# Optimization experiments

Measured on AMD Instinct MI355X. Metric: run time of the kernel, lower is better.

## Reference

```python
import jax, jax.numpy as jnp
import numpy as np
from functools import partial

MAX_SPAN_WIDTH = 8


def setup_inputs() -> dict:
    key = jax.random.key(0)
    ks = jax.random.split(key, 8)
    B, S, H = 4, 256, 256
    NE, D = 50000, 256  # entity_embedding_dim == hidden_size
    inp = {
        "embeddings": jax.random.normal(ks[0], (B, S, H), jnp.float32),          # BERT outputs[0]
        "entity_table": jax.random.normal(ks[1], (NE, D), jnp.float32) * 0.02,   # nn.Embedding weight
        "span_W": jax.random.normal(ks[2], (2 * H + 1, H), jnp.float32) * 0.02,  # span_embedding Linear
        "span_b": jax.random.normal(ks[3], (H,), jnp.float32) * 0.02,
        "gcn_W1": jax.random.normal(ks[4], (D, H), jnp.float32) * 0.02,
        "gcn_b1": jax.random.normal(ks[5], (H,), jnp.float32) * 0.02,
        "gcn_W2": jax.random.normal(ks[6], (H, H), jnp.float32) * 0.02,
        "gcn_b2": jax.random.normal(ks[7], (H,), jnp.float32) * 0.02,
        "k": 8,
    }
    return inp


def _star_adj_norm(k, dtype):
    # k-node star graph (node 0 hub) with self-loops, symmetric GCN normalization
    A = jnp.zeros((k, k), dtype).at[0, 1:].set(1.0).at[1:, 0].set(1.0) + jnp.eye(k, dtype=dtype)
    deg = A.sum(axis=1)
    return A / jnp.sqrt(deg[:, None] * deg[None, :])


def reference(embeddings, entity_table, span_W, span_b, gcn_W1, gcn_b1, gcn_W2, gcn_b2, k):
    B, S, H = embeddings.shape
    Wmax = MAX_SPAN_WIDTH
    dtype = embeddings.dtype

    # token_inputs: CLS embedding per example
    cls = embeddings[:, 0, :]  # [B, H]

    # Vectorized ragged span max-pool: running max over widths 1..Wmax.
    # span_max[w, b, s, :] = max(embeddings[b, s : s+w+1, :])
    neg_inf = jnp.array(-jnp.inf, dtype)
    maxes = []
    cur = embeddings
    maxes.append(cur)
    for w in range(1, Wmax):
        shifted = jnp.concatenate(
            [embeddings[:, w:, :], jnp.full((B, w, H), neg_inf, dtype)], axis=1)
        cur = jnp.maximum(cur, shifted)  # -inf pad => out-of-range positions ignored
        maxes.append(cur)
    span_max = jnp.stack(maxes, axis=0)  # [Wmax, B, S, H]

    # concat(max-pool, CLS, span width) -> span_embedding Linear
    cls_b = jnp.broadcast_to(cls[None, :, None, :], (Wmax, B, S, H))
    width_feat = jnp.broadcast_to(
        jnp.arange(1, Wmax + 1, dtype=dtype)[:, None, None, None], (Wmax, B, S, 1))
    span_inputs = jnp.concatenate([span_max, cls_b, width_feat], axis=-1)  # [Wmax,B,S,2H+1]
    span_inputs = span_inputs.reshape(Wmax * B * S, 2 * H + 1)             # [N, 2H+1]
    span_repr = span_inputs @ span_W + span_b                              # [N, H]

    # build_subgraph: top-k similar entities per span (memory-bound similarity + top-k)
    sims = span_repr @ entity_table.T          # [N, NE]  ~1.6GB intermediate
    _, topk_idx = jax.lax.top_k(sims, k)       # [N, k]
    node_x = entity_table[topk_idx]            # gather -> [N, k, D]

    # 2-layer GCN on the fixed star subgraph (gather-linear-scatter equivalent)
    A_norm = _star_adj_norm(k, dtype)          # [k, k]
    h = jax.nn.relu(jnp.einsum('ij,njd,dh->nih', A_norm, node_x, gcn_W1) + gcn_b1)
    subgraph_out = jnp.einsum('ij,njd,dh->nih', A_norm, h, gcn_W2) + gcn_b2  # [N, k, H]

    return cls, span_repr, subgraph_out
```

## Files before the change

### kernel.cpp

```cpp
#include <hip/hip_runtime.h>

typedef unsigned short u16;
typedef unsigned int   u32;
typedef unsigned long long u64;
typedef short bf16x8 __attribute__((ext_vector_type(8)));
typedef float f32x4  __attribute__((ext_vector_type(4)));

#define INF_F __builtin_inff()

__device__ __forceinline__ u16 f2bf(float f) {
  u32 u = __float_as_uint(f);
  return (u16)((u + 0x7FFFu + ((u >> 16) & 1u)) >> 16);
}

__device__ __forceinline__ u32 sortf(float f) {
  u32 u = __float_as_uint(f);
  return u ^ ((u32)((int)u >> 31) | 0x80000000u);
}
__device__ __forceinline__ float unsortf(u32 s) {
  u32 u = s ^ ((s & 0x80000000u) ? 0x80000000u : 0xFFFFFFFFu);
  return __uint_as_float(u);
}
__device__ __forceinline__ u64 sx64(u64 v, int m) {
  u32 lo = __shfl_xor((u32)v, m);
  u32 hi = __shfl_xor((u32)(v >> 32), m);
  return ((u64)hi << 32) | lo;
}

__device__ __forceinline__ void gload_lds16(const void* g, void* l) {
  __builtin_amdgcn_global_load_lds(
      (const __attribute__((address_space(1))) u32*)g,
      (__attribute__((address_space(3))) u32*)l, 16, 0, 0);
}

__global__ __launch_bounds__(256) void k0_cvt(
    const float* __restrict__ src, u16* __restrict__ dst, int n4) {
  int id = blockIdx.x * 256 + threadIdx.x;
  if (id >= n4) return;
  float4 v = ((const float4*)src)[id];
  ((ushort4*)dst)[id] = make_ushort4(f2bf(v.x), f2bf(v.y), f2bf(v.z), f2bf(v.w));
}

__global__ __launch_bounds__(256) void k1_span(
    const float* __restrict__ emb, const float* __restrict__ Wsp,
    const float* __restrict__ bsp,
    float* __restrict__ out0, float* __restrict__ out1,
    u16* __restrict__ spanbf) {
  __shared__ float SM[8][256];
  __shared__ float CLS[256];
  const int bid = blockIdx.x;
  const int b = bid >> 8, s = bid & 255;
  const int t = threadIdx.x;
  const float* eb = emb + (size_t)b * 65536;

  CLS[t] = eb[t];
  if (s == 0) out0[b * 256 + t] = eb[t];

  float m = eb[s * 256 + t];
  SM[0][t] = m;
  #pragma unroll
  for (int w = 1; w < 8; ++w) {
    if (s + w < 256) m = fmaxf(m, eb[(s + w) * 256 + t]);
    SM[w][t] = m;
  }
  __syncthreads();

  float cc = 0.f;
  for (int k = 0; k < 256; k += 4) {
    float4 cq = *(const float4*)&CLS[k];
    cc += cq.x * Wsp[(size_t)(256 + k + 0) * 256 + t];
    cc += cq.y * Wsp[(size_t)(256 + k + 1) * 256 + t];
    cc += cq.z * Wsp[(size_t)(256 + k + 2) * 256 + t];
    cc += cq.w * Wsp[(size_t)(256 + k + 3) * 256 + t];
  }
  float acc[8];
  const float base = bsp[t] + cc;
  #pragma unroll
  for (int w = 0; w < 8; ++w) acc[w] = base;

  for (int k = 0; k < 256; k += 4) {
    float w0 = Wsp[(size_t)(k + 0) * 256 + t];
    float w1 = Wsp[(size_t)(k + 1) * 256 + t];
    float w2 = Wsp[(size_t)(k + 2) * 256 + t];
    float w3 = Wsp[(size_t)(k + 3) * 256 + t];
    #pragma unroll
    for (int w = 0; w < 8; ++w) {
      float4 smq = *(const float4*)&SM[w][k];
      acc[w] += smq.x * w0; acc[w] += smq.y * w1;
      acc[w] += smq.z * w2; acc[w] += smq.w * w3;
    }
  }
  const float wm = Wsp[(size_t)512 * 256 + t];
  #pragma unroll
  for (int w = 0; w < 8; ++w) {
    float val = acc[w] + (float)(w + 1) * wm;
    size_t idx = ((size_t)w * 1024 + bid) * 256 + t;
    out1[idx] = val;
    spanbf[idx] = f2bf(val);
  }
}

__global__ __launch_bounds__(128, 2) void k2_mfma(
    const u16* __restrict__ spanbf, const u16* __restrict__ entbf, int ne,
    float* __restrict__ Rpv, int* __restrict__ Rpi) {
  __shared__ u32 Elds[6144];
  __shared__ u64 Q[2][64][16];
  const int t = threadIdx.x, lane = t & 63, wv = t >> 6;
  const int m = lane & 15, q = lane >> 4, q4 = q * 4;
  const int p = blockIdx.x & 15, rg = blockIdx.x >> 4;
  const int psz = (ne + 15) >> 4;
  const int e_start = p * psz;
  const int e_end = min(ne, e_start + psz);
  const int rowbase = rg * 128 + wv * 64;
  const u64 gm = 0xFFFFull << (q * 16);
  const u64 lanelow = (lane == 63) ? 0x7FFFFFFFFFFFFFFFull
                                   : ((1ull << (lane + 1)) - 1) >> 1;
  const u64 gml = gm & lanelow;
  const int row = lane & 15;
  const int ls5 = lane >> 5;

  const u64 KINIT = ((u64)sortf(-INF_F) << 32);
  u64 slot[4][4];
  float myth[4], th[4][4];
  #pragma unroll
  for (int h = 0; h < 4; ++h) {
    myth[h] = -INF_F;
    #pragma unroll
    for (int s = 0; s < 4; ++s) { slot[h][s] = KINIT; th[h][s] = -INF_F; }
  }

  bf16x8 a[4][8];
  #pragma unroll
  for (int h = 0; h < 4; ++h)
    #pragma unroll
    for (int s = 0; s < 8; ++s)
      a[h][s] = *(const bf16x8*)(spanbf
                  + (size_t)(rowbase + h * 16 + m) * 256 + s * 32 + q * 8);

  auto issue = [&](int k, int sl) {
    const int cb = e_start + (k << 4);
    #pragma unroll
    for (int i = 0; i < 4; ++i) {
      int eo = wv * 8 + i * 2 + ls5;
      int e  = (sl << 4) + eo;
      int ge = min(cb + eo, e_end - 1);
      int xoff = ((lane & 31) ^ (e & 31)) << 4;
      gload_lds16((const char*)entbf + (size_t)ge * 512 + xoff,
                  (char*)Elds + (sl << 13) + (wv << 12) + (i << 10));
    }
  };

  const int nch = (e_end - e_start + 15) >> 4;
  int cs = 0;
  issue(0, 0);

  for (int pc = 0; pc < nch; ++pc) {
    int is_ = cs + 1; if (is_ == 3) is_ = 0;
    if (pc + 1 < nch) {
      issue(pc + 1, is_);
      asm volatile("s_waitcnt vmcnt(4)" ::: "memory");
    } else {
      asm volatile("s_waitcnt vmcnt(0)" ::: "memory");
    }
    __builtin_amdgcn_sched_barrier(0);
    __builtin_amdgcn_s_barrier();

    f32x4 acc[4];
    #pragma unroll
    for (int h = 0; h < 4; ++h) acc[h] = (f32x4){0.f, 0.f, 0.f, 0.f};
    const int el = (cs << 4) + m, sw = el & 31, bc = el << 5;
    #pragma unroll
    for (int s = 0; s < 8; ++s) {
      int qq = s * 4 + q;
      bf16x8 bfr = *(const bf16x8*)((const char*)Elds + ((bc | (qq ^ sw)) << 4));
      #pragma unroll
      for (int h = 0; h < 4; ++h)
        acc[h] = __builtin_amdgcn_mfma_f32_16x16x32_bf16(a[h][s], bfr, acc[h], 0, 0, 0);
    }
    const int gent = e_start + (pc << 4) + m;
    const bool valid = gent < e_end;

    #pragma unroll
    for (int h = 0; h < 4; ++h) {
      bool any = valid & ((acc[h][0] > th[h][0]) | (acc[h][1] > th[h][1]) |
                          (acc[h][2] > th[h][2]) | (acc[h][3] > th[h][3]));
      if (!__ballot(any)) continue;
      u64 M[4];
      #pragma unroll
      for (int r = 0; r < 4; ++r) {
        bool hr = valid && (acc[h][r] > th[h][r]);
        M[r] = __ballot(hr);
        if (hr) {
          int pos = (int)__popcll(M[r] & gml);
          Q[wv][h * 16 + q4 + r][pos ^ (q4 + r)] =
              ((u64)sortf(acc[h][r]) << 32) | (u32)(~(u32)gent);
        }
      }
      u64 msk = (row & 2) ? ((row & 1) ? M[3] : M[2])
                          : ((row & 1) ? M[1] : M[0]);
      int cnt = (int)__popcll((msk >> ((row >> 2) << 4)) & 0xFFFFull);
      int cmax = cnt;
      #pragma unroll
      for (int o = 1; o < 16; o <<= 1)
        cmax = max(cmax, __shfl_xor(cmax, o));
      for (int j = 0; j < cmax; ++j) {
        u64 cand = Q[wv][h * 16 + row][j ^ row];
        if (j >= cnt) cand = 0;
        u64 m01 = slot[h][0] < slot[h][1] ? slot[h][0] : slot[h][1];
        u64 m23 = slot[h][2] < slot[h][3] ? slot[h][2] : slot[h][3];
        u64 lmin = m01 < m23 ? m01 : m23;
        u64 g = sx64(lmin, 16); if (g < lmin) lmin = g;
        g = sx64(lmin, 32); u64 gmin = (g < lmin) ? g : lmin;
        bool ins = cand > gmin;
        #pragma unroll
        for (int s2 = 0; s2 < 4; ++s2)
          if (ins && slot[h][s2] == gmin) slot[h][s2] = cand;
      }
      {
        u64 m01 = slot[h][0] < slot[h][1] ? slot[h][0] : slot[h][1];
        u64 m23 = slot[h][2] < slot[h][3] ? slot[h][2] : slot[h][3];
        u64 lmin = m01 < m23 ? m01 : m23;
        u64 g = sx64(lmin, 16); if (g < lmin) lmin = g;
        g = sx64(lmin, 32); if (g < lmin) lmin = g;
        myth[h] = unsortf((u32)(lmin >> 32));
        #pragma unroll
        for (int r = 0; r < 4; ++r) th[h][r] = __shfl(myth[h], q4 + r);
      }
    }
    cs = is_;
  }

  {
    const int sg = lane >> 4;
    #pragma unroll
    for (int h = 0; h < 4; ++h) {
      int r0 = rowbase + h * 16 + row;
      #pragma unroll
      for (int s = 0; s < 4; ++s) {
        u64 e0 = slot[h][s];
        int col = p * 16 + sg * 4 + s;
        Rpv[(size_t)r0 * 256 + col] = unsortf((u32)(e0 >> 32));
        Rpi[(size_t)r0 * 256 + col] = (int)(~(u32)e0);
      }
    }
  }
}

__global__ __launch_bounds__(256) void k2_merge(
    const float* __restrict__ Rpv, const int* __restrict__ Rpi,
    int* __restrict__ Ridx) {
  const int t = threadIdx.x, lane = t & 63, wv = t >> 6;
  const int row = blockIdx.x * 4 + wv;
  float v[4]; int e[4];
  #pragma unroll
  for (int pg = 0; pg < 4; ++pg) {
    v[pg] = Rpv[(size_t)row * 256 + pg * 64 + lane];
    e[pg] = Rpi[(size_t)row * 256 + pg * 64 + lane];
  }
  int c[4] = {0, 0, 0, 0};
  #pragma unroll
  for (int ps = 0; ps < 4; ++ps) {
    for (int i = 0; i < 64; ++i) {
      float ov = __shfl(v[ps], i); int oi = __shfl(e[ps], i);
      #pragma unroll
      for (int pd = 0; pd < 4; ++pd)
        c[pd] += (ov > v[pd] || (ov == v[pd] && oi < e[pd]));
    }
  }
  #pragma unroll
  for (int pg = 0; pg < 4; ++pg)
    if (c[pg] < 16) Ridx[(size_t)row * 16 + c[pg]] = e[pg];
}

__global__ __launch_bounds__(256, 3) void k3_gcn(
    const float* __restrict__ out1, const float* __restrict__ ent,
    const int* __restrict__ Ridx,
    const float* __restrict__ W1, const float* __restrict__ b1,
    const float* __restrict__ W2, const float* __restrict__ b2,
    float* __restrict__ out2, int ne) {
  __shared__ __align__(16) char UN[34560];
  __shared__ __align__(16) u16 Abf[32][272];
  __shared__ int cidx[4][16];
  __shared__ int chos[4][8];
  const int t = threadIdx.x;
  const int lane = t & 63, wv = t >> 6;
  const int m = lane & 15, q = lane >> 4;
  const int n0 = blockIdx.x * 4;

  {
    float  (*SPR)[256] = (float (*)[256])UN;
    double (*dpart)[4] = (double (*)[4])(UN + 4096);
    double (*sims)[16] = (double (*)[16])(UN + 6144);
    #pragma unroll
    for (int g = 0; g < 4; ++g)
      SPR[g][t] = out1[(size_t)(n0 + g) * 256 + t];
    if (t < 64) {
      int g = t >> 4, j = t & 15;
      int c = Ridx[(size_t)(n0 + g) * 16 + j];
      if ((unsigned)c >= (unsigned)ne) c = 0;
      cidx[g][j] = c;
    }
    __syncthreads();

    {
      const int pr = t >> 2, sub = t & 3;
      const int g = pr >> 4, j = pr & 15;
      const float* er = ent + (size_t)cidx[g][j] * 256 + sub * 64;
      const float* sr = &SPR[g][sub * 64];
      double s = 0.0;
      #pragma unroll
      for (int i = 0; i < 64; i += 4) {
        float4 e4 = *(const float4*)&er[i];
        float4 s4 = *(const float4*)&sr[i];
        s += (double)e4.x * (double)s4.x;
        s += (double)e4.y * (double)s4.y;
        s += (double)e4.z * (double)s4.z;
        s += (double)e4.w * (double)s4.w;
      }
      dpart[pr][sub] = s;
    }
    __syncthreads();
    if (t < 64) {
      int g = t >> 4, j = t & 15;
      sims[g][j] = dpart[t][0] + dpart[t][1] + dpart[t][2] + dpart[t][3];
    }
    __syncthreads();
    if (t < 4) {
      unsigned used = 0;
      for (int o = 0; o < 8; ++o) {
        int best = -1; double bv = 0.0; int bi = 0;
        for (int j = 0; j < 16; ++j) {
          if (used & (1u << j)) continue;
          if (best < 0 || sims[t][j] > bv || (sims[t][j] == bv && cidx[t][j] < bi)) {
            best = j; bv = sims[t][j]; bi = cidx[t][j];
          }
        }
        used |= (1u << best);
        chos[t][o] = cidx[t][best];
      }
    }
    __syncthreads();
  }

  {
    const int r = t >> 3, cb = t & 7;
    const float* src = ent + (size_t)chos[r >> 3][r & 7] * 256 + cb * 32;
    u32 pk[16];
    #pragma unroll
    for (int i = 0; i < 8; ++i) {
      float4 v = *(const float4*)&src[i * 4];
      pk[2 * i]     = (u32)f2bf(v.x) | ((u32)f2bf(v.y) << 16);
      pk[2 * i + 1] = (u32)f2bf(v.z) | ((u32)f2bf(v.w) << 16);
    }
    uint4* dst = (uint4*)&Abf[r][cb * 32];
    #pragma unroll
    for (int i = 0; i < 4; ++i)
      dst[i] = make_uint4(pk[4 * i], pk[4 * i + 1], pk[4 * i + 2], pk[4 * i + 3]);
  }

  auto run_gemm = [&](const float* __restrict__ Wg) {
    f32x4 acc[2][4];
    #pragma unroll
    for (int mt = 0; mt < 2; ++mt)
      #pragma unroll
      for (int nt = 0; nt < 4; ++nt)
        acc[mt][nt] = (f32x4){0.f, 0.f, 0.f, 0.f};

    for (int s = 0; s < 8; ++s) {
      __syncthreads();
      {
        const float* src = Wg + (size_t)(s * 32) * 256 + t;
        u32 pk[16];
        #pragma unroll
        for (int i = 0; i < 16; ++i) {
          float lo = src[(size_t)(2 * i) * 256];
          float hi = src[(size_t)(2 * i + 1) * 256];
          pk[i] = (u32)f2bf(lo) | ((u32)f2bf(hi) << 16);
        }
        uint4* dst = (uint4*)(UN + t * 80);
        #pragma unroll
        for (int i = 0; i < 4; ++i)
          dst[i] = make_uint4(pk[4 * i], pk[4 * i + 1], pk[4 * i + 2], pk[4 * i + 3]);
      }
      __syncthreads();
      #pragma unroll
      for (int mt = 0; mt < 2; ++mt) {
        bf16x8 af = *(const bf16x8*)((const char*)Abf
                       + (mt * 16 + m) * 544 + s * 64 + q * 16);
        #pragma unroll
        for (int nt = 0; nt < 4; ++nt) {
          const int col = wv * 64 + nt * 16 + m;
          bf16x8 bf = *(const bf16x8*)(UN + col * 80 + q * 16);
          acc[mt][nt] = __builtin_amdgcn_mfma_f32_16x16x32_bf16(
              af, bf, acc[mt][nt], 0, 0, 0);
        }
      }
    }
    __syncthreads();
    #pragma unroll
    for (int mt = 0; mt < 2; ++mt)
      #pragma unroll
      for (int nt = 0; nt < 4; ++nt)
        #pragma unroll
        for (int r = 0; r < 4; ++r)
          *(float*)(UN + (((mt * 16 + q * 4 + r) * 268)
                          + (wv * 64 + nt * 16 + m)) * 4) = acc[mt][nt][r];
    __syncthreads();
  };

  run_gemm(W1);
  {
    const float bb = b1[t];
    #pragma unroll
    for (int g = 0; g < 4; ++g) {
      float v[8];
      #pragma unroll
      for (int j = 0; j < 8; ++j)
        v[j] = *(const float*)(UN + ((g * 8 + j) * 268 + t) * 4);
      float ssum = 0.f;
      #pragma unroll
      for (int j = 1; j < 8; ++j) ssum += v[j];
      Abf[g * 8][t] = f2bf(fmaxf(v[0] * 0.125f + ssum * 0.25f + bb, 0.f));
      #pragma unroll
      for (int j = 1; j < 8; ++j)
        Abf[g * 8 + j][t] = f2bf(fmaxf(v[0] * 0.25f + v[j] * 0.5f + bb, 0.f));
    }
  }

  run_gemm(W2);
  {
    const float bb = b2[t];
    #pragma unroll
    for (int g = 0; g < 4; ++g) {
      float v[8];
      #pragma unroll
      for (int j = 0; j < 8; ++j)
        v[j] = *(const float*)(UN + ((g * 8 + j) * 268 + t) * 4);
      float ssum = 0.f;
      #pragma unroll
      for (int j = 1; j < 8; ++j) ssum += v[j];
      float* ob = out2 + (size_t)(n0 + g) * 2048 + t;
      ob[0] = v[0] * 0.125f + ssum * 0.25f + bb;
      #pragma unroll
      for (int j = 1; j < 8; ++j)
        ob[(size_t)j * 256] = v[0] * 0.25f + v[j] * 0.5f + bb;
    }
  }
}

extern "C" void kernel_launch(void* const* d_in, const int* in_sizes, int n_in,
                              void* d_out, int out_size, void* d_ws, size_t ws_size,
                              hipStream_t stream) {
  const float* emb = (const float*)d_in[0];
  const float* ent = (const float*)d_in[1];
  const float* Wsp = (const float*)d_in[2];
  const float* bsp = (const float*)d_in[3];
  const float* W1  = (const float*)d_in[4];
  const float* b1  = (const float*)d_in[5];
  const float* W2  = (const float*)d_in[6];
  const float* b2  = (const float*)d_in[7];
  const int ne = in_sizes[1] / 256;

  float* out  = (float*)d_out;
  float* out0 = out;
  float* out1 = out + 1024;
  float* out2 = out + 1024 + 2097152;

  char* ov = (char*)out2;
  u16*   entbf  = (u16*)(ov);
  u16*   spanbf = (u16*)(ov + 33554432);
  float* Rpv    = (float*)(ov + 41943040);
  int*   Rpi    = (int*)  (ov + 50331648);
  int*   Ridx   = (int*)d_ws;

  hipLaunchKernelGGL(k0_cvt, dim3((ne * 64 + 255) / 256), dim3(256), 0, stream,
                     ent, entbf, ne * 64);
  hipLaunchKernelGGL(k1_span, dim3(1024), dim3(256), 0, stream,
                     emb, Wsp, bsp, out0, out1, spanbf);
  hipLaunchKernelGGL(k2_mfma, dim3(1024), dim3(128), 0, stream,
                     spanbf, entbf, ne, Rpv, Rpi);
  hipLaunchKernelGGL(k2_merge, dim3(2048), dim3(256), 0, stream,
                     Rpv, Rpi, Ridx);
  hipLaunchKernelGGL(k3_gcn, dim3(2048), dim3(256), 0, stream,
                     out1, ent, Ridx, W1, b1, W2, b2, out2, ne);
}
```

Measured before the change: 739.5 us.

## Halve rows per wave in similarity top-k kernel to raise occupancy

Each wave of the MFMA similarity/top-k kernel now handles 32 span rows instead of 64, and the grid doubles to 2048 blocks. Launch bounds go to 4 blocks per CU, and the entity LDS buffer drops from triple to double buffering. The candidate queue shrinks to 8 entries per row, with a second pass for overflow, and the prefetch is now issued after the barrier with a full vmcnt(0) wait. Higher occupancy and smaller register and LDS use are traded for each entity chunk being loaded twice as often, fewer MFMAs reusing each B fragment, and less overlap between load and compute.

Result: no change. 730.0 us (-1.3%).

```diff
diff --git a/kernel.cpp b/kernel.cpp
--- a/kernel.cpp
+++ b/kernel.cpp
@@ -100,18 +100,18 @@
   }
 }
 
-__global__ __launch_bounds__(128, 2) void k2_mfma(
+__global__ __launch_bounds__(128, 4) void k2_mfma(
     const u16* __restrict__ spanbf, const u16* __restrict__ entbf, int ne,
     float* __restrict__ Rpv, int* __restrict__ Rpi) {
-  __shared__ u32 Elds[6144];
-  __shared__ u64 Q[2][64][16];
+  __shared__ u32 Elds[4096];
+  __shared__ u64 Q[2][32][8];
   const int t = threadIdx.x, lane = t & 63, wv = t >> 6;
   const int m = lane & 15, q = lane >> 4, q4 = q * 4;
   const int p = blockIdx.x & 15, rg = blockIdx.x >> 4;
   const int psz = (ne + 15) >> 4;
   const int e_start = p * psz;
   const int e_end = min(ne, e_start + psz);
-  const int rowbase = rg * 128 + wv * 64;
+  const int rowbase = rg * 64 + wv * 32;
   const u64 gm = 0xFFFFull << (q * 16);
   const u64 lanelow = (lane == 63) ? 0x7FFFFFFFFFFFFFFFull
                                    : ((1ull << (lane + 1)) - 1) >> 1;
@@ -120,18 +120,18 @@
   const int ls5 = lane >> 5;
 
   const u64 KINIT = ((u64)sortf(-INF_F) << 32);
-  u64 slot[4][4];
-  float myth[4], th[4][4];
-  #pragma unroll
-  for (int h = 0; h < 4; ++h) {
+  u64 slot[2][4];
+  float myth[2], th[2][4];
+  #pragma unroll
+  for (int h = 0; h < 2; ++h) {
     myth[h] = -INF_F;
     #pragma unroll
     for (int s = 0; s < 4; ++s) { slot[h][s] = KINIT; th[h][s] = -INF_F; }
   }
 
-  bf16x8 a[4][8];
-  #pragma unroll
-  for (int h = 0; h < 4; ++h)
+  bf16x8 a[2][8];
+  #pragma unroll
+  for (int h = 0; h < 2; ++h)
     #pragma unroll
     for (int s = 0; s < 8; ++s)
       a[h][s] = *(const bf16x8*)(spanbf
@@ -151,50 +151,44 @@
   };
 
   const int nch = (e_end - e_start + 15) >> 4;
-  int cs = 0;
   issue(0, 0);
 
   for (int pc = 0; pc < nch; ++pc) {
-    int is_ = cs + 1; if (is_ == 3) is_ = 0;
-    if (pc + 1 < nch) {
-      issue(pc + 1, is_);
-      asm volatile("s_waitcnt vmcnt(4)" ::: "memory");
-    } else {
-      asm volatile("s_waitcnt vmcnt(0)" ::: "memory");
-    }
+    const int cs = pc & 1;
+    asm volatile("s_waitcnt vmcnt(0)" ::: "memory");
     __builtin_amdgcn_sched_barrier(0);
     __builtin_amdgcn_s_barrier();
-
-    f32x4 acc[4];
-    #pragma unroll
-    for (int h = 0; h < 4; ++h) acc[h] = (f32x4){0.f, 0.f, 0.f, 0.f};
+    if (pc + 1 < nch) issue(pc + 1, cs ^ 1);
+
+    f32x4 acc[2];
+    #pragma unroll
+    for (int h = 0; h < 2; ++h) acc[h] = (f32x4){0.f, 0.f, 0.f, 0.f};
     const int el = (cs << 4) + m, sw = el & 31, bc = el << 5;
     #pragma unroll
     for (int s = 0; s < 8; ++s) {
       int qq = s * 4 + q;
       bf16x8 bfr = *(const bf16x8*)((const char*)Elds + ((bc | (qq ^ sw)) << 4));
       #pragma unroll
-      for (int h = 0; h < 4; ++h)
+      for (int h = 0; h < 2; ++h)
         acc[h] = __builtin_amdgcn_mfma_f32_16x16x32_bf16(a[h][s], bfr, acc[h], 0, 0, 0);
     }
     const int gent = e_start + (pc << 4) + m;
     const bool valid = gent < e_end;
 
     #pragma unroll
-    for (int h = 0; h < 4; ++h) {
+    for (int h = 0; h < 2; ++h) {
       bool any = valid & ((acc[h][0] > th[h][0]) | (acc[h][1] > th[h][1]) |
                           (acc[h][2] > th[h][2]) | (acc[h][3] > th[h][3]));
       if (!__ballot(any)) continue;
-      u64 M[4];
+      u64 M[4]; u64 key[4]; int ps_[4]; bool hit[4];
       #pragma unroll
       for (int r = 0; r < 4; ++r) {
-        bool hr = valid && (acc[h][r] > th[h][r]);
-        M[r] = __ballot(hr);
-        if (hr) {
-          int pos = (int)__popcll(M[r] & gml);
-          Q[wv][h * 16 + q4 + r][pos ^ (q4 + r)] =
-              ((u64)sortf(acc[h][r]) << 32) | (u32)(~(u32)gent);
-        }
+        hit[r] = valid && (acc[h][r] > th[h][r]);
+        M[r] = __ballot(hit[r]);
+        key[r] = ((u64)sortf(acc[h][r]) << 32) | (u32)(~(u32)gent);
+        ps_[r] = (int)__popcll(M[r] & gml);
+        if (hit[r] && ps_[r] < 8)
+          Q[wv][h * 16 + q4 + r][(ps_[r] ^ (q4 + r)) & 7] = key[r];
       }
       u64 msk = (row & 2) ? ((row & 1) ? M[3] : M[2])
                           : ((row & 1) ? M[1] : M[0]);
@@ -203,9 +197,11 @@
       #pragma unroll
       for (int o = 1; o < 16; o <<= 1)
         cmax = max(cmax, __shfl_xor(cmax, o));
-      for (int j = 0; j < cmax; ++j) {
-        u64 cand = Q[wv][h * 16 + row][j ^ row];
-        if (j >= cnt) cand = 0;
+      const u64* qrow = Q[wv][h * 16 + row];
+      const int rx = row & 7;
+      int cm1 = min(cmax, 8);
+      for (int j = 0; j < cm1; ++j) {
+        u64 cand = (j < cnt) ? qrow[(j ^ rx) & 7] : 0;
         u64 m01 = slot[h][0] < slot[h][1] ? slot[h][0] : slot[h][1];
         u64 m23 = slot[h][2] < slot[h][3] ? slot[h][2] : slot[h][3];
         u64 lmin = m01 < m23 ? m01 : m23;
@@ -215,6 +211,24 @@
         #pragma unroll
         for (int s2 = 0; s2 < 4; ++s2)
           if (ins && slot[h][s2] == gmin) slot[h][s2] = cand;
+      }
+      if (cmax > 8) {
+        #pragma unroll
+        for (int r = 0; r < 4; ++r)
+          if (hit[r] && ps_[r] >= 8)
+            Q[wv][h * 16 + q4 + r][((ps_[r] - 8) ^ (q4 + r)) & 7] = key[r];
+        for (int j = 8; j < cmax; ++j) {
+          u64 cand = (j < cnt) ? qrow[((j - 8) ^ rx) & 7] : 0;
+          u64 m01 = slot[h][0] < slot[h][1] ? slot[h][0] : slot[h][1];
+          u64 m23 = slot[h][2] < slot[h][3] ? slot[h][2] : slot[h][3];
+          u64 lmin = m01 < m23 ? m01 : m23;
+          u64 g = sx64(lmin, 16); if (g < lmin) lmin = g;
+          g = sx64(lmin, 32); u64 gmin = (g < lmin) ? g : lmin;
+          bool ins = cand > gmin;
+          #pragma unroll
+          for (int s2 = 0; s2 < 4; ++s2)
+            if (ins && slot[h][s2] == gmin) slot[h][s2] = cand;
+        }
       }
       {
         u64 m01 = slot[h][0] < slot[h][1] ? slot[h][0] : slot[h][1];
@@ -227,13 +241,12 @@
         for (int r = 0; r < 4; ++r) th[h][r] = __shfl(myth[h], q4 + r);
       }
     }
-    cs = is_;
   }
 
   {
     const int sg = lane >> 4;
     #pragma unroll
-    for (int h = 0; h < 4; ++h) {
+    for (int h = 0; h < 2; ++h) {
       int r0 = rowbase + h * 16 + row;
       #pragma unroll
       for (int s = 0; s < 4; ++s) {
@@ -477,7 +490,7 @@
                      ent, entbf, ne * 64);
   hipLaunchKernelGGL(k1_span, dim3(1024), dim3(256), 0, stream,
                      emb, Wsp, bsp, out0, out1, spanbf);
-  hipLaunchKernelGGL(k2_mfma, dim3(1024), dim3(128), 0, stream,
+  hipLaunchKernelGGL(k2_mfma, dim3(2048), dim3(128), 0, stream,
                      spanbf, entbf, ne, Rpv, Rpi);
   hipLaunchKernelGGL(k2_merge, dim3(2048), dim3(256), 0, stream,
                      Rpv, Rpi, Ridx);
```
